# Performance work log

Measured on AMD Instinct MI355X. Metric: run time of the kernel, lower is better.

The kernel has to match this reference:

```python
import jax, jax.numpy as jnp
import numpy as np
import math

B, S, E, H, D = 2, 2048, 1024, 16, 64

def setup_inputs() -> dict:
    key = jax.random.key(0)
    ks = jax.random.split(key, 9)
    sc = 0.02
    return {
        "x": jax.random.normal(ks[0], (B, S, E), jnp.float32),
        "Wq": jax.random.normal(ks[1], (H, E, D), jnp.float32) * sc,
        "Wk": jax.random.normal(ks[2], (H, E, D), jnp.float32) * sc,
        "Wv": jax.random.normal(ks[3], (H, E, D), jnp.float32) * sc,
        "bq": jax.random.normal(ks[4], (H, D), jnp.float32) * sc,
        "bk": jax.random.normal(ks[5], (H, D), jnp.float32) * sc,
        "bv": jax.random.normal(ks[6], (H, D), jnp.float32) * sc,
        "Wo": jax.random.normal(ks[7], (H * D, E), jnp.float32) * sc,
        "bo": jax.random.normal(ks[8], (E,), jnp.float32) * sc,
    }

def reference(x, Wq, Wk, Wv, bq, bk, bv, Wo, bo):
    # per-head projections, batched over heads: [B,H,S,D]
    q = jnp.einsum('bse,hed->bhsd', x, Wq) + bq[None, :, None, :]
    k = jnp.einsum('bse,hed->bhsd', x, Wk) + bk[None, :, None, :]
    v = jnp.einsum('bse,hed->bhsd', x, Wv) + bv[None, :, None, :]
    # full score matrix [B,H,S,S], scaled by sqrt(head_size) as in original
    scores = jnp.einsum('bhqd,bhkd->bhqk', q, k) / math.sqrt(D)
    causal = jnp.tril(jnp.ones((S, S), bool))  # tril mask as in buffer
    scores = jnp.where(causal[None, None], scores, -jnp.inf)
    attn = jax.nn.softmax(scores, axis=-1)
    out = jnp.einsum('bhqk,bhkd->bhqd', attn, v)
    # concat heads in head order: [B,S,H*D]
    out = out.transpose(0, 2, 1, 3).reshape(B, S, H * D)
    # output projection (dropout is identity in eval / p=0)
    return out @ Wo + bo
```

## Files before the change

kernel.cpp:

```cpp
#include <hip/hip_runtime.h>

#define BB 2
#define SS 2048
#define EE 1024
#define HH 16
#define DD 64

typedef unsigned short u16;
typedef float f4 __attribute__((ext_vector_type(4)));
typedef __bf16 b8 __attribute__((ext_vector_type(8)));
typedef short s8i __attribute__((ext_vector_type(8)));
typedef u16 u16x4 __attribute__((ext_vector_type(4)));

__device__ inline u16 f2b(float f) {
  unsigned u = __builtin_bit_cast(unsigned, f);
  unsigned r = (u + 0x7fffu + ((u >> 16) & 1u)) >> 16;
  return (u16)r;
}

__global__ __launch_bounds__(256) void prep(const float* __restrict__ x,
                                            const float* __restrict__ Wq,
                                            const float* __restrict__ Wk,
                                            const float* __restrict__ Wv,
                                            const float* __restrict__ Wo,
                                            u16* __restrict__ xb,
                                            u16* __restrict__ Wt,
                                            u16* __restrict__ Wot) {
  int bid = blockIdx.x;
  int t = threadIdx.x;
  if (bid < 1024) {
    int i0 = bid * 256 + t;
    for (int j = 0; j < 4; ++j) {
      int i = i0 + j * 262144;
      f4 v = ((const f4*)x)[i];
      u16x4 o;
      for (int k2 = 0; k2 < 4; ++k2) o[k2] = f2b(v[k2]);
      ((u16x4*)xb)[i] = o;
    }
  } else if (bid < 1792) {
    __shared__ float tile[64][65];
    int z = bid - 1024;
    int y = z >> 4;
    int e0 = (z & 15) * 64;
    int qkv = y >> 4, h = y & 15;
    const float* W = (qkv == 0) ? Wq : (qkv == 1) ? Wk : Wv;
    for (int p = 0; p < 16; ++p) {
      int i = p * 4 + (t >> 6), d = t & 63;
      tile[i][d] = W[((size_t)h * EE + e0 + i) * DD + d];
    }
    __syncthreads();
    for (int p = 0; p < 16; ++p) {
      int d = p * 4 + (t >> 6), i = t & 63;
      Wt[((size_t)qkv * 1024 + h * 64 + d) * EE + e0 + i] = f2b(tile[i][d]);
    }
  } else {
    __shared__ float tile2[64][65];
    int z = bid - 1792;
    int e0 = (z & 15) * 64, c0 = (z >> 4) * 64;
    for (int p = 0; p < 16; ++p) {
      int i = p * 4 + (t >> 6), j = t & 63;
      tile2[i][j] = Wo[(size_t)(e0 + i) * (HH * DD) + c0 + j];
    }
    __syncthreads();
    for (int p = 0; p < 16; ++p) {
      int j = p * 4 + (t >> 6), i = t & 63;
      Wot[(size_t)(c0 + j) * EE + e0 + i] = f2b(tile2[i][j]);
    }
  }
}

__global__ __launch_bounds__(256) void gemmQKV(
    const u16* __restrict__ xb, const u16* __restrict__ Wt,
    u16* __restrict__ Qo, u16* __restrict__ Ko, u16* __restrict__ Vo,
    const float* __restrict__ bq, const float* __restrict__ bk,
    const float* __restrict__ bv) {
  const int K = 1024;
  __shared__ u16 SM[8192];
  u16* As = SM;
  u16* Bs = SM + 4096;
  int t = threadIdx.x;
  int lane = t & 63, w = t >> 6;
  int wr = w >> 1, wc = w & 1;
  int lr = lane & 15, lg = lane >> 4;

  int bid = blockIdx.x;
  bool isV = bid >= 512;
  int m0, n0;
  const u16 *Ap, *Bp;
  if (!isV) {
    m0 = (bid >> 4) * 128;
    n0 = (bid & 15) * 128;
    Ap = xb;
    Bp = Wt;
  } else {
    int z = bid - 512;
    m0 = (z >> 5) * 128;
    n0 = (z & 31) * 128;
    Ap = Wt + (size_t)2048 * 1024;
    Bp = xb;
  }

  f4 acc[4][4];
  const f4 z4 = {0.f, 0.f, 0.f, 0.f};
  for (int mi = 0; mi < 4; ++mi)
    for (int ni = 0; ni < 4; ++ni) acc[mi][ni] = z4;

  int r0 = t >> 2, s0 = t & 3;
  const u16* ga0 = Ap + (size_t)(m0 + r0) * K + s0 * 8;
  const u16* gb0 = Bp + (size_t)(n0 + r0) * K + s0 * 8;
  u16* la0 = As + w * 512;
  u16* la1 = As + 2048 + w * 512;
  u16* lb0 = Bs + w * 512;
  u16* lb1 = Bs + 2048 + w * 512;

  for (int ks = 0; ks < K / 32; ++ks) {
    int k0 = ks * 32;
    __builtin_amdgcn_global_load_lds(
        (const __attribute__((address_space(1))) void*)(ga0 + k0),
        (__attribute__((address_space(3))) void*)la0, 16, 0, 0);
    __builtin_amdgcn_global_load_lds(
        (const __attribute__((address_space(1))) void*)(ga0 + 64 * K + k0),
        (__attribute__((address_space(3))) void*)la1, 16, 0, 0);
    __builtin_amdgcn_global_load_lds(
        (const __attribute__((address_space(1))) void*)(gb0 + k0),
        (__attribute__((address_space(3))) void*)lb0, 16, 0, 0);
    __builtin_amdgcn_global_load_lds(
        (const __attribute__((address_space(1))) void*)(gb0 + 64 * K + k0),
        (__attribute__((address_space(3))) void*)lb1, 16, 0, 0);
    __syncthreads();
    b8 af[4], bf[4];
    for (int mi = 0; mi < 4; ++mi)
      af[mi] = *(const b8*)&As[(wr * 64 + mi * 16 + lr) * 32 + lg * 8];
    for (int ni = 0; ni < 4; ++ni)
      bf[ni] = *(const b8*)&Bs[(wc * 64 + ni * 16 + lr) * 32 + lg * 8];
    for (int mi = 0; mi < 4; ++mi)
      for (int ni = 0; ni < 4; ++ni)
        acc[mi][ni] = __builtin_amdgcn_mfma_f32_16x16x32_bf16(af[mi], bf[ni],
                                                              acc[mi][ni], 0, 0, 0);
    __syncthreads();
  }

  const float QSC = 0.18033688011112042f;
  u16(*SMv)[128] = (u16(*)[128])SM;
  for (int hh = 0; hh < 2; ++hh) {
    __syncthreads();
    if (wr == hh) {
      for (int mi = 0; mi < 4; ++mi)
        for (int ni = 0; ni < 4; ++ni)
          for (int r = 0; r < 4; ++r) {
            int lrow = mi * 16 + lg * 4 + r;
            int lcol = wc * 64 + ni * 16 + lr;
            float v = acc[mi][ni][r];
            if (!isV) {
              int n_g = n0 + lcol;
              int qkv = n_g >> 10, hd = n_g & 1023;
              v += (qkv == 0) ? bq[hd] : bk[hd];
              if (qkv == 0) v *= QSC;
            } else {
              v += bv[m0 + hh * 64 + lrow];
            }
            SMv[lrow][lcol] = f2b(v);
          }
    }
    __syncthreads();
    if (!isV) {
      int b = m0 >> 11;
      int sbase = (m0 & 2047) + hh * 64;
      for (int q = 0; q < 4; ++q) {
        int c = t + q * 256;
        int h_i = c >> 9, row = (c >> 3) & 63, slot = c & 7;
        int n_g = n0 + h_i * 64;
        int qkv = n_g >> 10, hd = n_g & 1023;
        int h = hd >> 6;
        u16* dst = (qkv == 0) ? Qo : Ko;
        *(s8i*)(dst + (((size_t)b * HH + h) * SS + sbase + row) * DD + slot * 8) =
            *(const s8i*)&SMv[row][h_i * 64 + slot * 8];
      }
    } else {
      int b = n0 >> 11;
      int scol = n0 & 2047;
      int h = (m0 + hh * 64) >> 6;
      int dbase = (m0 + hh * 64) & 63;
      for (int q = 0; q < 4; ++q) {
        int c = t + q * 256;
        int row = c >> 4, slot = c & 15;
        *(s8i*)(Vo + (((size_t)b * HH + h) * DD + dbase + row) * SS + scol + slot * 8) =
            *(const s8i*)&SMv[row][slot * 8];
      }
    }
  }
}

__global__ __launch_bounds__(256) void gemmO(const u16* __restrict__ A,
                                             const u16* __restrict__ Bm,
                                             float* __restrict__ Co,
                                             const float* __restrict__ bo) {
  const int K = 1024;
  __shared__ u16 As[128 * 32];
  __shared__ u16 Bs[64 * 32];
  __shared__ float Sf[64 * 64];
  int t = threadIdx.x;
  int lane = t & 63, w = t >> 6;
  int lr = lane & 15, lg = lane >> 4;
  int m0 = blockIdx.y * 128, n0 = blockIdx.x * 64;

  f4 acc[2][4];
  const f4 z4 = {0.f, 0.f, 0.f, 0.f};
  for (int mi = 0; mi < 2; ++mi)
    for (int ni = 0; ni < 4; ++ni) acc[mi][ni] = z4;

  int r0 = t >> 2, s0 = t & 3;
  const u16* ga0 = A + (size_t)(m0 + r0) * K + s0 * 8;
  const u16* gb0 = Bm + (size_t)(n0 + r0) * K + s0 * 8;
  u16* la0 = As + w * 512;
  u16* la1 = As + 2048 + w * 512;
  u16* lb0 = Bs + w * 512;

  for (int ks = 0; ks < K / 32; ++ks) {
    int k0 = ks * 32;
    __builtin_amdgcn_global_load_lds(
        (const __attribute__((address_space(1))) void*)(ga0 + k0),
        (__attribute__((address_space(3))) void*)la0, 16, 0, 0);
    __builtin_amdgcn_global_load_lds(
        (const __attribute__((address_space(1))) void*)(ga0 + 64 * K + k0),
        (__attribute__((address_space(3))) void*)la1, 16, 0, 0);
    __builtin_amdgcn_global_load_lds(
        (const __attribute__((address_space(1))) void*)(gb0 + k0),
        (__attribute__((address_space(3))) void*)lb0, 16, 0, 0);
    __syncthreads();
    b8 af[2], bf[4];
    for (int mi = 0; mi < 2; ++mi)
      af[mi] = *(const b8*)&As[(w * 32 + mi * 16 + lr) * 32 + lg * 8];
    for (int ni = 0; ni < 4; ++ni)
      bf[ni] = *(const b8*)&Bs[(ni * 16 + lr) * 32 + lg * 8];
    for (int mi = 0; mi < 2; ++mi)
      for (int ni = 0; ni < 4; ++ni)
        acc[mi][ni] = __builtin_amdgcn_mfma_f32_16x16x32_bf16(af[mi], bf[ni],
                                                              acc[mi][ni], 0, 0, 0);
    __syncthreads();
  }

  for (int hh = 0; hh < 2; ++hh) {
    __syncthreads();
    if ((w >> 1) == hh) {
      for (int mi = 0; mi < 2; ++mi)
        for (int ni = 0; ni < 4; ++ni)
          for (int r = 0; r < 4; ++r) {
            int lrow = (w & 1) * 32 + mi * 16 + lg * 4 + r;
            int lcol = ni * 16 + lr;
            Sf[lrow * 64 + lcol] = acc[mi][ni][r] + bo[n0 + lcol];
          }
    }
    __syncthreads();
    for (int q = 0; q < 4; ++q) {
      int c = t + q * 256;
      int row = c >> 4, slot = c & 15;
      *(f4*)(Co + (size_t)(m0 + hh * 64 + row) * 1024 + n0 + slot * 4) =
          *(const f4*)&Sf[row * 64 + slot * 4];
    }
  }
}

#define KST 72
#define PST 72
__global__ __launch_bounds__(512) void fattn(const u16* __restrict__ Qb,
                                             const u16* __restrict__ Kb,
                                             const u16* __restrict__ VTb,
                                             u16* __restrict__ AO) {
  __shared__ u16 Kl[2][64 * KST];
  __shared__ u16 Vl[2][64 * KST];
  __shared__ u16 Pl[8][16 * PST];

  int t = threadIdx.x, lane = t & 63, w = t >> 6;
  int lr = lane & 15, lg = lane >> 4;
  int id = blockIdx.x;
  int bh = id & 31;
  int p = id >> 5;
  int qb = (p < 8) ? (15 - p) : (p - 8);
  int b = bh >> 4, h = bh & 15;
  size_t base = (size_t)bh * SS * DD;

  int r0 = t >> 3, s0 = t & 7;
  int s0p = s0 ^ (r0 & 7);
  u16* kl0 = &Kl[0][r0 * KST + s0p * 8];
  u16* kl1 = &Kl[1][r0 * KST + s0p * 8];
  u16* vl0 = &Vl[0][r0 * KST + s0p * 8];
  u16* vl1 = &Vl[1][r0 * KST + s0p * 8];
  const u16* kg = Kb + base + (size_t)r0 * DD + s0 * 8;
  const u16* vg = VTb + base + (size_t)r0 * SS + s0 * 8;

  int qbase = qb * 128;
  int nt = 2 * qb + 2;

  const u16* qp = Qb + base + (size_t)(qbase + w * 16 + lr) * DD;
  b8 qf0 = *(const b8*)(qp + lg * 8);
  b8 qf1 = *(const b8*)(qp + 32 + lg * 8);

  const f4 z4 = {0.f, 0.f, 0.f, 0.f};
  f4 o[4];
  for (int i = 0; i < 4; ++i) o[i] = z4;
  float mrow[4], lsum[4];
  for (int r = 0; r < 4; ++r) { mrow[r] = -1e30f; lsum[r] = 0.f; }
  int qg = qbase + w * 16 + lg * 4;

  int fsl = lg ^ (lr & 7);

  *(s8i*)kl0 = *(const s8i*)kg;
  *(s8i*)vl0 = *(const s8i*)vg;
  __syncthreads();

  for (int kt = 0; kt < nt; ++kt) {
    int cur = kt & 1;
    int kv0 = kt * 64;

    s8i nk, nv;
    bool more = (kt + 1 < nt);
    if (more) {
      nk = *(const s8i*)(kg + (size_t)(kv0 + 64) * DD);
      nv = *(const s8i*)(vg + kv0 + 64);
    }

    f4 sa[4];
    for (int n = 0; n < 4; ++n) sa[n] = z4;
    for (int n = 0; n < 4; ++n) {
      const u16* krow = &Kl[cur][(n * 16 + lr) * KST];
      b8 kf0 = *(const b8*)(krow + fsl * 8);
      b8 kf1 = *(const b8*)(krow + (fsl ^ 4) * 8);
      sa[n] = __builtin_amdgcn_mfma_f32_16x16x32_bf16(qf0, kf0, sa[n], 0, 0, 0);
      sa[n] = __builtin_amdgcn_mfma_f32_16x16x32_bf16(qf1, kf1, sa[n], 0, 0, 0);
    }

    if (kt >= nt - 2) {
      for (int r = 0; r < 4; ++r) {
        int q = qg + r;
        if (kv0 + lr > q) sa[0][r] = -1e30f;
        if (kv0 + 16 + lr > q) sa[1][r] = -1e30f;
        if (kv0 + 32 + lr > q) sa[2][r] = -1e30f;
        if (kv0 + 48 + lr > q) sa[3][r] = -1e30f;
      }
    }

    float scl[4];
    for (int r = 0; r < 4; ++r) {
      float mx = fmaxf(fmaxf(sa[0][r], sa[1][r]), fmaxf(sa[2][r], sa[3][r]));
      mx = fmaxf(mx, __shfl_xor(mx, 1));
      mx = fmaxf(mx, __shfl_xor(mx, 2));
      mx = fmaxf(mx, __shfl_xor(mx, 4));
      mx = fmaxf(mx, __shfl_xor(mx, 8));
      float mn = fmaxf(mrow[r], mx);
      float sc = __builtin_amdgcn_exp2f(mrow[r] - mn);
      float p0 = __builtin_amdgcn_exp2f(sa[0][r] - mn);
      float p1 = __builtin_amdgcn_exp2f(sa[1][r] - mn);
      float p2 = __builtin_amdgcn_exp2f(sa[2][r] - mn);
      float p3 = __builtin_amdgcn_exp2f(sa[3][r] - mn);
      lsum[r] = lsum[r] * sc + ((p0 + p1) + (p2 + p3));
      mrow[r] = mn;
      scl[r] = sc;
      int prow = (lg * 4 + r) * PST;
      Pl[w][prow + lr] = f2b(p0);
      Pl[w][prow + 16 + lr] = f2b(p1);
      Pl[w][prow + 32 + lr] = f2b(p2);
      Pl[w][prow + 48 + lr] = f2b(p3);
    }
    for (int n = 0; n < 4; ++n) {
      f4 ov = o[n];
      for (int r = 0; r < 4; ++r) ov[r] *= scl[r];
      o[n] = ov;
    }

    b8 pf0 = *(const b8*)&Pl[w][lr * PST + lg * 8];
    b8 pf1 = *(const b8*)&Pl[w][lr * PST + 32 + lg * 8];
    for (int n = 0; n < 4; ++n) {
      const u16* vrow = &Vl[cur][(n * 16 + lr) * KST];
      b8 vf0 = *(const b8*)(vrow + fsl * 8);
      b8 vf1 = *(const b8*)(vrow + (fsl ^ 4) * 8);
      o[n] = __builtin_amdgcn_mfma_f32_16x16x32_bf16(pf0, vf0, o[n], 0, 0, 0);
      o[n] = __builtin_amdgcn_mfma_f32_16x16x32_bf16(pf1, vf1, o[n], 0, 0, 0);
    }

    if (more) {
      *(s8i*)(cur ? kl0 : kl1) = nk;
      *(s8i*)(cur ? vl0 : vl1) = nv;
    }
    __syncthreads();
  }

  float rl[4];
  for (int r = 0; r < 4; ++r) {
    float s = lsum[r];
    s += __shfl_xor(s, 1);
    s += __shfl_xor(s, 2);
    s += __shfl_xor(s, 4);
    s += __shfl_xor(s, 8);
    rl[r] = 1.f / s;
  }
  for (int n = 0; n < 4; ++n)
    for (int r = 0; r < 4; ++r) {
      int qgr = qg + r;
      int d = n * 16 + lr;
      AO[((size_t)b * SS + qgr) * (HH * DD) + h * DD + d] = f2b(o[n][r] * rl[r]);
    }
}

extern "C" void kernel_launch(void* const* d_in, const int* in_sizes, int n_in,
                              void* d_out, int out_size, void* d_ws, size_t ws_size,
                              hipStream_t stream) {
  const float* x  = (const float*)d_in[0];
  const float* Wq = (const float*)d_in[1];
  const float* Wk = (const float*)d_in[2];
  const float* Wv = (const float*)d_in[3];
  const float* bq = (const float*)d_in[4];
  const float* bk = (const float*)d_in[5];
  const float* bv = (const float*)d_in[6];
  const float* Wo = (const float*)d_in[7];
  const float* bo = (const float*)d_in[8];

  char* ws = (char*)d_ws;
  u16* xb  = (u16*)(ws);
  u16* Wt  = (u16*)(ws + ((size_t)8 << 20));
  u16* Wot = (u16*)(ws + ((size_t)14 << 20));
  u16* Qw  = (u16*)(ws + ((size_t)16 << 20));
  u16* Kw  = (u16*)(ws + ((size_t)24 << 20));
  u16* VTw = (u16*)(ws + ((size_t)32 << 20));
  u16* AO  = xb;

  prep<<<2048, 256, 0, stream>>>(x, Wq, Wk, Wv, Wo, xb, Wt, Wot);
  gemmQKV<<<768, 256, 0, stream>>>(xb, Wt, Qw, Kw, VTw, bq, bk, bv);
  fattn<<<512, 512, 0, stream>>>(Qw, Kw, VTw, AO);
  gemmO<<<dim3(16, 32), 256, 0, stream>>>(AO, Wot, (float*)d_out, bo);
}
```

Before: 235.7 us.

## Remap GEMM block order for XCD locality, enlarge gemmO tile, drop K/V LDS swizzle

gemmQKV and gemmO now permute block IDs so that consecutive blocks landing on the same XCD (bid&7) share input panels, aiming for better L2 reuse. gemmO moves from 128x64 to 128x128 tiles with a 2x2 wave layout and a 1D grid of 256 blocks, doubling the MFMA work per block and reducing redundant A loads. In fattn, the XOR swizzle on K/V shared-memory stores and fragment reads is removed in favour of plain padded (stride 72) indexing, which simplifies address math. The trade-offs are possible bank conflicts in attention and fewer gemmO blocks (256) to fill the GPU's compute units.

Result: no change. 240.3 us (+1.9%).

```diff
diff --git a/kernel.cpp b/kernel.cpp
--- a/kernel.cpp
+++ b/kernel.cpp
@@ -84,18 +84,19 @@
   int lr = lane & 15, lg = lane >> 4;
 
   int bid = blockIdx.x;
-  bool isV = bid >= 512;
+  int work = (bid & 7) * 96 + (bid >> 3);
+  bool isV = work >= 512;
   int m0, n0;
   const u16 *Ap, *Bp;
   if (!isV) {
-    m0 = (bid >> 4) * 128;
-    n0 = (bid & 15) * 128;
+    m0 = (work & 31) * 128;
+    n0 = (work >> 5) * 128;
     Ap = xb;
     Bp = Wt;
   } else {
-    int z = bid - 512;
-    m0 = (z >> 5) * 128;
-    n0 = (z & 31) * 128;
+    int z = work - 512;
+    m0 = (z & 7) * 128;
+    n0 = (z >> 3) * 128;
     Ap = Wt + (size_t)2048 * 1024;
     Bp = xb;
   }
@@ -197,16 +198,19 @@
                                              const float* __restrict__ bo) {
   const int K = 1024;
   __shared__ u16 As[128 * 32];
-  __shared__ u16 Bs[64 * 32];
-  __shared__ float Sf[64 * 64];
+  __shared__ u16 Bs[128 * 32];
+  __shared__ float Sf[32 * 128];
   int t = threadIdx.x;
   int lane = t & 63, w = t >> 6;
+  int wr = w >> 1, wc = w & 1;
   int lr = lane & 15, lg = lane >> 4;
-  int m0 = blockIdx.y * 128, n0 = blockIdx.x * 64;
-
-  f4 acc[2][4];
+  int bid = blockIdx.x;
+  int work = (bid & 7) * 32 + (bid >> 3);
+  int m0 = (work & 31) * 128, n0 = (work >> 5) * 128;
+
+  f4 acc[4][4];
   const f4 z4 = {0.f, 0.f, 0.f, 0.f};
-  for (int mi = 0; mi < 2; ++mi)
+  for (int mi = 0; mi < 4; ++mi)
     for (int ni = 0; ni < 4; ++ni) acc[mi][ni] = z4;
 
   int r0 = t >> 2, s0 = t & 3;
@@ -215,6 +219,7 @@
   u16* la0 = As + w * 512;
   u16* la1 = As + 2048 + w * 512;
   u16* lb0 = Bs + w * 512;
+  u16* lb1 = Bs + 2048 + w * 512;
 
   for (int ks = 0; ks < K / 32; ++ks) {
     int k0 = ks * 32;
@@ -227,36 +232,40 @@
     __builtin_amdgcn_global_load_lds(
         (const __attribute__((address_space(1))) void*)(gb0 + k0),
         (__attribute__((address_space(3))) void*)lb0, 16, 0, 0);
-    __syncthreads();
-    b8 af[2], bf[4];
-    for (int mi = 0; mi < 2; ++mi)
-      af[mi] = *(const b8*)&As[(w * 32 + mi * 16 + lr) * 32 + lg * 8];
+    __builtin_amdgcn_global_load_lds(
+        (const __attribute__((address_space(1))) void*)(gb0 + 64 * K + k0),
+        (__attribute__((address_space(3))) void*)lb1, 16, 0, 0);
+    __syncthreads();
+    b8 af[4], bf[4];
+    for (int mi = 0; mi < 4; ++mi)
+      af[mi] = *(const b8*)&As[(wr * 64 + mi * 16 + lr) * 32 + lg * 8];
     for (int ni = 0; ni < 4; ++ni)
-      bf[ni] = *(const b8*)&Bs[(ni * 16 + lr) * 32 + lg * 8];
-    for (int mi = 0; mi < 2; ++mi)
+      bf[ni] = *(const b8*)&Bs[(wc * 64 + ni * 16 + lr) * 32 + lg * 8];
+    for (int mi = 0; mi < 4; ++mi)
       for (int ni = 0; ni < 4; ++ni)
         acc[mi][ni] = __builtin_amdgcn_mfma_f32_16x16x32_bf16(af[mi], bf[ni],
                                                               acc[mi][ni], 0, 0, 0);
     __syncthreads();
   }
 
-  for (int hh = 0; hh < 2; ++hh) {
-    __syncthreads();
-    if ((w >> 1) == hh) {
-      for (int mi = 0; mi < 2; ++mi)
+  for (int hh = 0; hh < 4; ++hh) {
+    __syncthreads();
+    if (wr == (hh >> 1)) {
+      int mi0 = (hh & 1) * 2;
+      for (int mi = mi0; mi < mi0 + 2; ++mi)
         for (int ni = 0; ni < 4; ++ni)
           for (int r = 0; r < 4; ++r) {
-            int lrow = (w & 1) * 32 + mi * 16 + lg * 4 + r;
-            int lcol = ni * 16 + lr;
-            Sf[lrow * 64 + lcol] = acc[mi][ni][r] + bo[n0 + lcol];
+            int lrow = (mi - mi0) * 16 + lg * 4 + r;
+            int lcol = wc * 64 + ni * 16 + lr;
+            Sf[lrow * 128 + lcol] = acc[mi][ni][r] + bo[n0 + lcol];
           }
     }
     __syncthreads();
     for (int q = 0; q < 4; ++q) {
       int c = t + q * 256;
-      int row = c >> 4, slot = c & 15;
-      *(f4*)(Co + (size_t)(m0 + hh * 64 + row) * 1024 + n0 + slot * 4) =
-          *(const f4*)&Sf[row * 64 + slot * 4];
+      int row = c >> 5, slot = c & 31;
+      *(f4*)(Co + (size_t)(m0 + hh * 32 + row) * 1024 + n0 + slot * 4) =
+          *(const f4*)&Sf[row * 128 + slot * 4];
     }
   }
 }
@@ -281,11 +290,10 @@
   size_t base = (size_t)bh * SS * DD;
 
   int r0 = t >> 3, s0 = t & 7;
-  int s0p = s0 ^ (r0 & 7);
-  u16* kl0 = &Kl[0][r0 * KST + s0p * 8];
-  u16* kl1 = &Kl[1][r0 * KST + s0p * 8];
-  u16* vl0 = &Vl[0][r0 * KST + s0p * 8];
-  u16* vl1 = &Vl[1][r0 * KST + s0p * 8];
+  u16* kl0 = &Kl[0][r0 * KST + s0 * 8];
+  u16* kl1 = &Kl[1][r0 * KST + s0 * 8];
+  u16* vl0 = &Vl[0][r0 * KST + s0 * 8];
+  u16* vl1 = &Vl[1][r0 * KST + s0 * 8];
   const u16* kg = Kb + base + (size_t)r0 * DD + s0 * 8;
   const u16* vg = VTb + base + (size_t)r0 * SS + s0 * 8;
 
@@ -303,8 +311,6 @@
   for (int r = 0; r < 4; ++r) { mrow[r] = -1e30f; lsum[r] = 0.f; }
   int qg = qbase + w * 16 + lg * 4;
 
-  int fsl = lg ^ (lr & 7);
-
   *(s8i*)kl0 = *(const s8i*)kg;
   *(s8i*)vl0 = *(const s8i*)vg;
   __syncthreads();
@@ -324,8 +330,8 @@
     for (int n = 0; n < 4; ++n) sa[n] = z4;
     for (int n = 0; n < 4; ++n) {
       const u16* krow = &Kl[cur][(n * 16 + lr) * KST];
-      b8 kf0 = *(const b8*)(krow + fsl * 8);
-      b8 kf1 = *(const b8*)(krow + (fsl ^ 4) * 8);
+      b8 kf0 = *(const b8*)(krow + lg * 8);
+      b8 kf1 = *(const b8*)(krow + 32 + lg * 8);
       sa[n] = __builtin_amdgcn_mfma_f32_16x16x32_bf16(qf0, kf0, sa[n], 0, 0, 0);
       sa[n] = __builtin_amdgcn_mfma_f32_16x16x32_bf16(qf1, kf1, sa[n], 0, 0, 0);
     }
@@ -372,8 +378,8 @@
     b8 pf1 = *(const b8*)&Pl[w][lr * PST + 32 + lg * 8];
     for (int n = 0; n < 4; ++n) {
       const u16* vrow = &Vl[cur][(n * 16 + lr) * KST];
-      b8 vf0 = *(const b8*)(vrow + fsl * 8);
-      b8 vf1 = *(const b8*)(vrow + (fsl ^ 4) * 8);
+      b8 vf0 = *(const b8*)(vrow + lg * 8);
+      b8 vf1 = *(const b8*)(vrow + 32 + lg * 8);
       o[n] = __builtin_amdgcn_mfma_f32_16x16x32_bf16(pf0, vf0, o[n], 0, 0, 0);
       o[n] = __builtin_amdgcn_mfma_f32_16x16x32_bf16(pf1, vf1, o[n], 0, 0, 0);
     }
@@ -427,5 +433,5 @@
   prep<<<2048, 256, 0, stream>>>(x, Wq, Wk, Wv, Wo, xb, Wt, Wot);
   gemmQKV<<<768, 256, 0, stream>>>(xb, Wt, Qw, Kw, VTw, bq, bk, bv);
   fattn<<<512, 512, 0, stream>>>(Qw, Kw, VTw, AO);
-  gemmO<<<dim3(16, 32), 256, 0, stream>>>(AO, Wot, (float*)d_out, bo);
-}
+  gemmO<<<256, 256, 0, stream>>>(AO, Wot, (float*)d_out, bo);
+}
```
